# Optimization experiments

Hardware: AMD Instinct MI355X
Metric: run time of the kernel (lower is better)

Reference implementation:

```python
import jax, jax.numpy as jnp
import numpy as np

NU, NI, NR = 50000, 50000, 5   # users, items, rating levels
D, B, LS, LI = 64, 512, 32, 64 # embed_dim, batch, max social nbrs, max item hist
NEG = -1e9


def setup_inputs() -> dict:
    key = jax.random.key(0)
    ks = iter(jax.random.split(key, 64))
    def lin(din, dout):
        s = 1.0 / np.sqrt(din)
        return (jax.random.uniform(next(ks), (din, dout), minval=-s, maxval=s, dtype=jnp.float32),
                jax.random.uniform(next(ks), (dout,), minval=-s, maxval=s, dtype=jnp.float32))
    inp = {}
    inp['user_w'] = jax.random.normal(next(ks), (NU, D), dtype=jnp.float32) * 0.1
    inp['item_w'] = jax.random.normal(next(ks), (NI, D), dtype=jnp.float32) * 0.1
    inp['rating_w'] = jax.random.normal(next(ks), (NR, D), dtype=jnp.float32) * 0.1
    for name, din, dout in [('i_ln1', 2*D, D), ('i_ln2', D, D), ('i_ln3', 2*D, D),
                            ('i_att1', 2*D, D), ('i_att2', D, D), ('i_att3', D, 1),
                            ('s_ln1', D, D), ('s_ln2', 2*D, D), ('s_ln3', D, D),
                            ('s_att1', 2*D, D), ('s_att2', D, D), ('s_att3', D, 1)]:
        w, b = lin(din, dout)
        inp[name + '_w'] = w
        inp[name + '_b'] = b
    inp['nodes'] = jax.random.randint(next(ks), (B,), 0, NU)
    inp['social_hist'] = jax.random.randint(next(ks), (NU, LS), 0, NU)
    inp['social_mask'] = jax.random.bernoulli(next(ks), 0.5, (NU, LS)).at[:, 0].set(True)
    inp['item_hist'] = jax.random.randint(next(ks), (NU, LI), 0, NI)
    inp['rating_hist'] = jax.random.randint(next(ks), (NU, LI), 0, NR)
    inp['item_mask'] = jax.random.bernoulli(next(ks), 0.5, (NU, LI)).at[:, 0].set(True)
    return inp


def reference(user_w, item_w, rating_w,
              i_ln1_w, i_ln1_b, i_ln2_w, i_ln2_b, i_ln3_w, i_ln3_b,
              i_att1_w, i_att1_b, i_att2_w, i_att2_b, i_att3_w, i_att3_b,
              s_ln1_w, s_ln1_b, s_ln2_w, s_ln2_b, s_ln3_w, s_ln3_b,
              s_att1_w, s_att1_b, s_att2_w, s_att2_b, s_att3_w, s_att3_b,
              nodes, social_hist, social_mask, item_hist, rating_hist, item_mask):
    relu = jax.nn.relu

    def attn(x, w1, b1, w2, b2, w3, b3, mask):
        # x: [..., L, 2D] -> softmax weights over valid neighbors: [..., L]
        h = relu(x @ w1 + b1)
        h = relu(h @ w2 + b2)
        logit = (h @ w3 + b3)[..., 0]
        logit = jnp.where(mask, logit, NEG)
        return jax.nn.softmax(logit, axis=-1)

    def item_final(uids):
        # uids: any shape [...]; returns [..., D]  (Aggre_item.item_final)
        its, rts, m = item_hist[uids], rating_hist[uids], item_mask[uids]
        x = jnp.concatenate([item_w[its], rating_w[rts]], axis=-1)   # [...,LI,2D]
        x = relu(x @ i_ln1_w + i_ln1_b)                              # [...,LI,D]
        u = user_w[uids]                                             # [...,D]
        a_in = jnp.concatenate([x, jnp.broadcast_to(u[..., None, :], x.shape)], axis=-1)
        alpha = attn(a_in, i_att1_w, i_att1_b, i_att2_w, i_att2_b, i_att3_w, i_att3_b, m)
        hI = jnp.einsum('...l,...ld->...d', alpha, x)                # attention-weighted sum
        hI = relu(hI @ i_ln2_w + i_ln2_b)
        return relu(jnp.concatenate([u, hI], axis=-1) @ i_ln3_w + i_ln3_b)

    # item-space factor of query users
    hI_self = item_final(nodes)                                      # [B,D]
    # social aggregation: item_final over each user's social neighbors
    nbrs, nmask = social_hist[nodes], social_mask[nodes]             # [B,LS]
    hI_nb = item_final(nbrs)                                         # [B,LS,D]
    u = user_w[nodes]                                                # [B,D]
    b_in = jnp.concatenate([hI_nb, jnp.broadcast_to(u[:, None, :], hI_nb.shape)], axis=-1)
    beta = attn(b_in, s_att1_w, s_att1_b, s_att2_w, s_att2_b, s_att3_w, s_att3_b, nmask)
    hS = jnp.einsum('bl,bld->bd', beta, hI_nb)
    hS = relu(hS @ s_ln1_w + s_ln1_b)
    f = jnp.concatenate([hI_self, hS], axis=-1)
    f = relu(f @ s_ln2_w + s_ln2_b)
    return relu(f @ s_ln3_w + s_ln3_b)
```

## Files before the change

kernel.cpp:

```cpp
#include <hip/hip_runtime.h>
#include <math.h>


#define NII 50000
#define BB 512
#define LSS 32
#define NT 16896

typedef short short8 __attribute__((ext_vector_type(8)));
typedef float f32x4 __attribute__((ext_vector_type(4)));

static __device__ __forceinline__ bool mread(const void* p, long i, int mode) {
  if (mode == 0) return ((const int*)p)[i] != 0;
  if (mode == 2) return ((const float*)p)[i] != 0.0f;
  return ((const unsigned char*)p)[i] != 0;
}

static __device__ __forceinline__ float wsum(float v) {
#pragma unroll
  for (int s = 1; s < 64; s <<= 1) v += __shfl_xor(v, s);
  return v;
}
static __device__ __forceinline__ float wmax(float v) {
#pragma unroll
  for (int s = 1; s < 64; s <<= 1) v = fmaxf(v, __shfl_xor(v, s));
  return v;
}
static __device__ __forceinline__ float rsum16(float v) {
#pragma unroll
  for (int s = 1; s < 16; s <<= 1) v += __shfl_xor(v, s);
  return v;
}

static __device__ __forceinline__ short bf16rne(float f) {
  unsigned u = __float_as_uint(f);
  u = (u + 0x7FFFu + ((u >> 16) & 1u)) >> 16;
  return (short)u;
}
static __device__ __forceinline__ float bf16tof(short h) {
  return __uint_as_float(((unsigned)(unsigned short)h) << 16);
}

static __device__ __forceinline__ void wave_fence() {
  asm volatile("s_waitcnt lgkmcnt(0)" ::: "memory");
  __builtin_amdgcn_sched_barrier(0);
}

__global__ void setup_kernel(const unsigned int* __restrict__ sm,
                             int* __restrict__ flag,
                             const float* __restrict__ rating_w,
                             const float* __restrict__ w1,
                             const float* __restrict__ b1,
                             float* __restrict__ RW1g,
                             const float* __restrict__ A1w,
                             const float* __restrict__ A2w,
                             short* __restrict__ B1,
                             short* __restrict__ B2,
                             short* __restrict__ W1hi,
                             short* __restrict__ W1lo,
                             const int* __restrict__ nodes,
                             const int* __restrict__ social_hist,
                             int* __restrict__ counter,
                             int* __restrict__ list,
                             int* __restrict__ aUid) {
  const int tid = threadIdx.x;
  if (blockIdx.x == 0) {
    __shared__ int notInt, notFloat;
    if (tid == 0) { notInt = 0; notFloat = 0; }
    __syncthreads();
    int ni = 0, nf = 0;
    for (int i = tid; i < 4096; i += 256) {
      unsigned int x = sm[i];
      if (x > 1u) ni = 1;
      if (x != 0u && x != 0x3F800000u) nf = 1;
    }
    if (ni) atomicOr(&notInt, 1);
    if (nf) atomicOr(&notFloat, 1);
    __syncthreads();
    if (tid == 0) flag[0] = notInt ? (notFloat ? 1 : 2) : 0;
  } else if (blockIdx.x == 1) {
    for (int t = tid; t < 320; t += 256) {
      const int r = t >> 6, c = t & 63;
      float acc = b1[c];
      for (int k = 0; k < 64; ++k)
        acc = fmaf(rating_w[r * 64 + k], w1[(64 + k) * 64 + c], acc);
      RW1g[r * 64 + c] = acc;
    }
  } else if (blockIdx.x == 2) {
    for (int idx = tid; idx < 4096; idx += 256) {
      int e = idx & 7, g = idx >> 3;
      int l = g & 63, q = g >> 6;
      int kb = q >> 2, nb = q & 3;
      int k = kb * 32 + ((l >> 4) & 3) * 8 + e;
      int col = nb * 16 + (l & 15);
      B1[idx] = bf16rne(A1w[k * 64 + col]);
      B2[idx] = bf16rne(A2w[k * 64 + col]);
      float a = w1[k * 64 + col];
      short h = bf16rne(a);
      W1hi[idx] = h;
      W1lo[idx] = bf16rne(a - bf16tof(h));
    }
  } else {
    __shared__ int nI, nF;
    if (tid == 0) { nI = 0; nF = 0; }
    __syncthreads();
    int ni = 0, nf = 0;
    for (int i = tid; i < 4096; i += 256) {
      unsigned int x = sm[i];
      if (x > 1u) ni = 1;
      if (x != 0u && x != 0x3F800000u) nf = 1;
    }
    if (ni) atomicOr(&nI, 1);
    if (nf) atomicOr(&nF, 1);
    __syncthreads();
    const int mode = nI ? (nF ? 1 : 2) : 0;
    const int t = (blockIdx.x - 3) * 256 + tid;
    if (t < NT) {
      int uid;
      bool active;
      if (t < BB) {
        active = true;
        uid = nodes[t];
      } else {
        int nb = t - BB;
        int b = nb >> 5, l = nb & 31;
        long mi = (long)nodes[b] * LSS + l;
        active = mread((const void*)sm, mi, mode);
        uid = active ? social_hist[mi] : 0;
      }
      if (active) {
        int pos = atomicAdd(counter, 1);
        list[pos] = t;
        aUid[pos] = uid;
      }
    }
  }
}

__global__ __launch_bounds__(256)
void pre_xbase_mfma_kernel(const float* __restrict__ item_w,
                           const short* __restrict__ W1hi,
                           const short* __restrict__ W1lo,
                           float* __restrict__ xbase) {
  const int lane = threadIdx.x & 63, w = threadIdx.x >> 6;
  const int l15 = lane & 15, lg4 = lane >> 4;
  short8 bh[8], bl[8];
#pragma unroll
  for (int q = 0; q < 8; ++q) {
    bh[q] = *(const short8*)(W1hi + (q * 64 + lane) * 8);
    bl[q] = *(const short8*)(W1lo + (q * 64 + lane) * 8);
  }
  const int wid = blockIdx.x * 4 + w;
  const int nw = gridDim.x * 4;
  for (int tile = wid; tile < 3125; tile += nw) {
    const long r0 = (long)tile * 16;
    const float* ap = item_w + (r0 + l15) * 64 + lg4 * 8;
    short8 ah[2], al[2];
#pragma unroll
    for (int kb = 0; kb < 2; ++kb) {
      const float4 a = *(const float4*)(ap + kb * 32);
      const float4 b = *(const float4*)(ap + kb * 32 + 4);
      float v[8] = {a.x, a.y, a.z, a.w, b.x, b.y, b.z, b.w};
      short8 hi, lo;
#pragma unroll
      for (int e = 0; e < 8; ++e) {
        short h = bf16rne(v[e]);
        hi[e] = h;
        lo[e] = bf16rne(v[e] - bf16tof(h));
      }
      ah[kb] = hi;
      al[kb] = lo;
    }
#pragma unroll
    for (int nb = 0; nb < 4; ++nb) {
      f32x4 acc = {0.0f, 0.0f, 0.0f, 0.0f};
      acc = __builtin_amdgcn_mfma_f32_16x16x32_bf16(ah[0], bh[0 * 4 + nb], acc, 0, 0, 0);
      acc = __builtin_amdgcn_mfma_f32_16x16x32_bf16(ah[1], bh[1 * 4 + nb], acc, 0, 0, 0);
      acc = __builtin_amdgcn_mfma_f32_16x16x32_bf16(ah[0], bl[0 * 4 + nb], acc, 0, 0, 0);
      acc = __builtin_amdgcn_mfma_f32_16x16x32_bf16(ah[1], bl[1 * 4 + nb], acc, 0, 0, 0);
      acc = __builtin_amdgcn_mfma_f32_16x16x32_bf16(al[0], bh[0 * 4 + nb], acc, 0, 0, 0);
      acc = __builtin_amdgcn_mfma_f32_16x16x32_bf16(al[1], bh[1 * 4 + nb], acc, 0, 0, 0);
#pragma unroll
      for (int r = 0; r < 4; ++r)
        xbase[(r0 + lg4 * 4 + r) * 64 + nb * 16 + l15] = acc[r];
    }
  }
}

__global__ __launch_bounds__(256, 2)
void uA1_kernel(const float* __restrict__ user_w,
                const float* __restrict__ A1w, const float* __restrict__ A1b,
                const int* __restrict__ idxsrc, const int* __restrict__ nActp,
                float* __restrict__ uA1buf) {
  const int tid = threadIdx.x, lane = tid & 63, w = tid >> 6;
  const int i0 = blockIdx.x * 64;
  const int nA = nActp[0];
  if (i0 >= nA) return;
  __shared__ float sW[64][64], sU[64][64];
  __shared__ float sb[64];
  __shared__ int sUid[64];
  for (int i = tid; i < 4096; i += 256) sW[i >> 6][i & 63] = A1w[4096 + i];
  if (tid < 64) {
    sb[tid] = A1b[tid];
    sUid[tid] = (i0 + tid < nA) ? idxsrc[i0 + tid] : 0;
  }
  __syncthreads();
  for (int i = tid; i < 4096; i += 256) {
    int r = i >> 6, c = i & 63;
    sU[r][c] = user_w[(long)sUid[r] * 64 + c];
  }
  __syncthreads();
  float acc[16];
#pragma unroll
  for (int r = 0; r < 16; ++r) acc[r] = sb[lane];
  for (int k = 0; k < 64; k += 4) {
    float wv0 = sW[k][lane], wv1 = sW[k + 1][lane];
    float wv2 = sW[k + 2][lane], wv3 = sW[k + 3][lane];
#pragma unroll
    for (int r = 0; r < 16; ++r) {
      const float4 xv = *(const float4*)(&sU[w * 16 + r][k]);
      acc[r] = fmaf(xv.x, wv0, acc[r]);
      acc[r] = fmaf(xv.y, wv1, acc[r]);
      acc[r] = fmaf(xv.z, wv2, acc[r]);
      acc[r] = fmaf(xv.w, wv3, acc[r]);
    }
  }
#pragma unroll
  for (int r = 0; r < 16; ++r) {
    int row = i0 + w * 16 + r;
    if (row < nA) uA1buf[(long)row * 64 + lane] = acc[r];
  }
}

__global__ __launch_bounds__(512, 8)
void core_mfma_kernel(const float* __restrict__ xbase,
                      const float* __restrict__ RW1g,
                      const float* __restrict__ uA1buf,
                      const short* __restrict__ Bimg1,
                      const short* __restrict__ Bimg2,
                      const float* __restrict__ A2b,
                      const float* __restrict__ A3w,
                      const int* __restrict__ item_hist,
                      const int* __restrict__ rating_hist,
                      const void* __restrict__ item_mask,
                      const int* __restrict__ flagp,
                      const int* __restrict__ aUid,
                      const int* __restrict__ nActp,
                      float* __restrict__ hvecbuf) {
  __shared__ __align__(16) short sB1[4096], sB2[4096];
  __shared__ __align__(16) char smem[8][3072];
  const int tid = threadIdx.x, lane = tid & 63, w = tid >> 6;
  const int nA = nActp[0];
  if (blockIdx.x * 8 >= nA) return;

  short* h1w = (short*)(smem[w]);
  float* lgw = (float*)(smem[w] + 2560);
  int* cw = (int*)(smem[w] + 2816);

  ((int4*)sB1)[tid] = ((const int4*)Bimg1)[tid];
  ((int4*)sB2)[tid] = ((const int4*)Bimg2)[tid];
  __syncthreads();

  const int idx = blockIdx.x * 8 + w;
  if (idx >= nA) return;

  const int mode = flagp[0];
  const float a2bv = A2b[lane];
  const float a3v = A3w[lane];
  const int l15 = lane & 15;
  const int lg4 = lane >> 4;

#define B1F(q) (*(const short8*)(sB1 + ((q) * 64 + lane) * 8))
#define B2F(q) (*(const short8*)(sB2 + ((q) * 64 + lane) * 8))

  const long uid = aUid[idx];

  const long mbase = uid * 64;
  bool mk = mread(item_mask, mbase + lane, mode);
  unsigned long long bal = __ballot(mk);
  const int nact = (int)__popcll(bal);
  int pos = (int)__popcll(bal & ((1ull << lane) - 1ull));
  if (mk) cw[pos] = (item_hist[mbase + lane] << 3) | rating_hist[mbase + lane];
  const float uA1v = uA1buf[(long)idx * 64 + lane];
  wave_fence();

  const int ng = (nact + 15) >> 4;
  for (int mc = 0; mc < ng; ++mc) {
    wave_fence();
    int row = mc * 16 + l15;
    if (row >= nact) row = nact - 1;
    const int p = cw[row];
    const long it = p >> 3;
    const int rt = p & 7;
    short8 xa[2];
#pragma unroll
    for (int kb = 0; kb < 2; ++kb) {
      const int koff = kb * 32 + lg4 * 8;
      const float* xp = xbase + it * 64 + koff;
      const float* rp = RW1g + rt * 64 + koff;
      const float4 a = *(const float4*)xp;
      const float4 b = *(const float4*)(xp + 4);
      const float4 c = *(const float4*)rp;
      const float4 d = *(const float4*)(rp + 4);
      short8 f;
      f[0] = bf16rne(fmaxf(a.x + c.x, 0.0f));
      f[1] = bf16rne(fmaxf(a.y + c.y, 0.0f));
      f[2] = bf16rne(fmaxf(a.z + c.z, 0.0f));
      f[3] = bf16rne(fmaxf(a.w + c.w, 0.0f));
      f[4] = bf16rne(fmaxf(b.x + d.x, 0.0f));
      f[5] = bf16rne(fmaxf(b.y + d.y, 0.0f));
      f[6] = bf16rne(fmaxf(b.z + d.z, 0.0f));
      f[7] = bf16rne(fmaxf(b.w + d.w, 0.0f));
      xa[kb] = f;
    }
#pragma unroll
    for (int nb = 0; nb < 4; ++nb) {
      const float ui = __shfl(uA1v, nb * 16 + l15);
      f32x4 acc = {ui, ui, ui, ui};
      acc = __builtin_amdgcn_mfma_f32_16x16x32_bf16(xa[0], B1F(0 * 4 + nb), acc, 0, 0, 0);
      acc = __builtin_amdgcn_mfma_f32_16x16x32_bf16(xa[1], B1F(1 * 4 + nb), acc, 0, 0, 0);
#pragma unroll
      for (int r = 0; r < 4; ++r)
        h1w[(lg4 * 4 + r) * 80 + nb * 16 + l15] = bf16rne(fmaxf(acc[r], 0.0f));
    }
    wave_fence();
    short8 ha[2];
    ha[0] = *(const short8*)(h1w + l15 * 80 + lg4 * 8);
    ha[1] = *(const short8*)(h1w + l15 * 80 + 32 + lg4 * 8);
    float t0 = 0.0f, t1 = 0.0f, t2 = 0.0f, t3 = 0.0f;
#pragma unroll
    for (int nb = 0; nb < 4; ++nb) {
      const float b2 = __shfl(a2bv, nb * 16 + l15);
      f32x4 acc = {b2, b2, b2, b2};
      acc = __builtin_amdgcn_mfma_f32_16x16x32_bf16(ha[0], B2F(0 * 4 + nb), acc, 0, 0, 0);
      acc = __builtin_amdgcn_mfma_f32_16x16x32_bf16(ha[1], B2F(1 * 4 + nb), acc, 0, 0, 0);
      const float a3c = __shfl(a3v, nb * 16 + l15);
      t0 = fmaf(fmaxf(acc[0], 0.0f), a3c, t0);
      t1 = fmaf(fmaxf(acc[1], 0.0f), a3c, t1);
      t2 = fmaf(fmaxf(acc[2], 0.0f), a3c, t2);
      t3 = fmaf(fmaxf(acc[3], 0.0f), a3c, t3);
    }
    t0 = rsum16(t0); t1 = rsum16(t1); t2 = rsum16(t2); t3 = rsum16(t3);
    if (l15 == 0) {
      const int jb = mc * 16 + lg4 * 4;
      lgw[jb + 0] = t0;
      lgw[jb + 1] = t1;
      lgw[jb + 2] = t2;
      lgw[jb + 3] = t3;
    }
  }
  wave_fence();

  const bool valid = (lane < nact);
  float lv = valid ? lgw[lane] : -1e30f;
  float mx = wmax(lv);
  float e = valid ? __expf(lv - mx) : 0.0f;
  float s = wsum(e);
  const float alpha = e / s;

  float h0 = 0.0f, hA = 0.0f, hB = 0.0f, hC = 0.0f;
  int j = 0;
  for (; j + 3 < nact; j += 4) {
    const int p0 = cw[j], p1 = cw[j + 1], p2 = cw[j + 2], p3 = cw[j + 3];
    const float a0 = __shfl(alpha, j), a1 = __shfl(alpha, j + 1);
    const float a2 = __shfl(alpha, j + 2), a3 = __shfl(alpha, j + 3);
    const float x0 = xbase[(long)(p0 >> 3) * 64 + lane] + RW1g[(p0 & 7) * 64 + lane];
    const float x1 = xbase[(long)(p1 >> 3) * 64 + lane] + RW1g[(p1 & 7) * 64 + lane];
    const float x2 = xbase[(long)(p2 >> 3) * 64 + lane] + RW1g[(p2 & 7) * 64 + lane];
    const float x3 = xbase[(long)(p3 >> 3) * 64 + lane] + RW1g[(p3 & 7) * 64 + lane];
    h0 = fmaf(a0, fmaxf(x0, 0.0f), h0);
    hA = fmaf(a1, fmaxf(x1, 0.0f), hA);
    hB = fmaf(a2, fmaxf(x2, 0.0f), hB);
    hC = fmaf(a3, fmaxf(x3, 0.0f), hC);
  }
  for (; j < nact; ++j) {
    const int p = cw[j];
    const float aj = __shfl(alpha, j);
    const float xv = xbase[(long)(p >> 3) * 64 + lane] + RW1g[(p & 7) * 64 + lane];
    h0 = fmaf(aj, fmaxf(xv, 0.0f), h0);
  }
  hvecbuf[(long)idx * 64 + lane] = (h0 + hA) + (hB + hC);
#undef B1F
#undef B2F
}

__global__ __launch_bounds__(256, 2)
void hI2final_kernel(const float* __restrict__ hvecbuf,
                     const float* __restrict__ user_w,
                     const float* __restrict__ W2w, const float* __restrict__ W2b,
                     const float* __restrict__ W3w, const float* __restrict__ W3b,
                     const int* __restrict__ list, const int* __restrict__ aUid,
                     const int* __restrict__ nActp, float* __restrict__ hIbuf) {
  const int tid = threadIdx.x, lane = tid & 63, w = tid >> 6;
  const int i0 = blockIdx.x * 32;
  const int nA = nActp[0];
  if (i0 >= nA) return;
  __shared__ float sW[128][64];
  __shared__ float sX[32][128];
  __shared__ float sb[64];
  __shared__ int sUid[32], sInst[32];
  for (int i = tid; i < 4096; i += 256) sW[i >> 6][i & 63] = W2w[i];
  if (tid < 64) sb[tid] = W2b[tid];
  if (tid < 32) {
    bool ok = (i0 + tid) < nA;
    sUid[tid] = ok ? aUid[i0 + tid] : 0;
    sInst[tid] = ok ? list[i0 + tid] : 0;
  }
  __syncthreads();
  for (int i = tid; i < 2048; i += 256) {
    int r = i >> 6, c = i & 63;
    sX[r][64 + c] = (i0 + r < nA) ? hvecbuf[(long)(i0 + r) * 64 + c] : 0.0f;
    sX[r][c] = user_w[(long)sUid[r] * 64 + c];
  }
  __syncthreads();

  float acc[8];
  {
    const float bv = sb[lane];
#pragma unroll
    for (int r = 0; r < 8; ++r) acc[r] = bv;
    for (int k = 0; k < 64; k += 4) {
      float wv0 = sW[k][lane], wv1 = sW[k + 1][lane];
      float wv2 = sW[k + 2][lane], wv3 = sW[k + 3][lane];
#pragma unroll
      for (int r = 0; r < 8; ++r) {
        const float4 xv = *(const float4*)(&sX[w * 8 + r][64 + k]);
        acc[r] = fmaf(xv.x, wv0, acc[r]);
        acc[r] = fmaf(xv.y, wv1, acc[r]);
        acc[r] = fmaf(xv.z, wv2, acc[r]);
        acc[r] = fmaf(xv.w, wv3, acc[r]);
      }
    }
#pragma unroll
    for (int r = 0; r < 8; ++r) sX[w * 8 + r][64 + lane] = fmaxf(acc[r], 0.0f);
  }
  __syncthreads();
  for (int i = tid; i < 8192; i += 256) sW[i >> 6][i & 63] = W3w[i];
  if (tid < 64) sb[tid] = W3b[tid];
  __syncthreads();

  {
    const float bv = sb[lane];
#pragma unroll
    for (int r = 0; r < 8; ++r) acc[r] = bv;
    for (int k = 0; k < 128; k += 4) {
      float wv0 = sW[k][lane], wv1 = sW[k + 1][lane];
      float wv2 = sW[k + 2][lane], wv3 = sW[k + 3][lane];
#pragma unroll
      for (int r = 0; r < 8; ++r) {
        const float4 xv = *(const float4*)(&sX[w * 8 + r][k]);
        acc[r] = fmaf(xv.x, wv0, acc[r]);
        acc[r] = fmaf(xv.y, wv1, acc[r]);
        acc[r] = fmaf(xv.z, wv2, acc[r]);
        acc[r] = fmaf(xv.w, wv3, acc[r]);
      }
    }
#pragma unroll
    for (int r = 0; r < 8; ++r) {
      int row = i0 + w * 8 + r;
      if (row < nA)
        hIbuf[(long)sInst[w * 8 + r] * 64 + lane] = fmaxf(acc[r], 0.0f);
    }
  }
}

__global__ __launch_bounds__(256, 8)
void social_fused_kernel(const float* __restrict__ hIbuf,
                         const float* __restrict__ user_w,
                         const float* __restrict__ S1w,
                         const float* __restrict__ S1b,
                         const float* __restrict__ S2w,
                         const float* __restrict__ S2b,
                         const float* __restrict__ S3w,
                         const float* __restrict__ L1w, const float* __restrict__ L1b,
                         const float* __restrict__ L2w, const float* __restrict__ L2b,
                         const float* __restrict__ L3w, const float* __restrict__ L3b,
                         const int* __restrict__ nodes,
                         const void* __restrict__ social_mask,
                         const int* __restrict__ flagp,
                         float* __restrict__ out) {
  __shared__ __align__(16) short sB1[4096], sB2[4096];
  __shared__ __align__(16) char smem[4][3584];
  const int tid = threadIdx.x, lane = tid & 63, w = tid >> 6;
  short* h1w = (short*)(smem[w]);
  float* lgw = (float*)(smem[w] + 2560);
  int* cw = (int*)(smem[w] + 2816);
  float* vA = (float*)(smem[w] + 3072);
  float* vB = (float*)(smem[w] + 3328);

  for (int i = tid; i < 4096; i += 256) {
    int e = i & 7, g = i >> 3;
    int l = g & 63, q = g >> 6;
    int kb = q >> 2, nb = q & 3;
    int k = kb * 32 + ((l >> 4) & 3) * 8 + e;
    int col = nb * 16 + (l & 15);
    sB1[i] = bf16rne(S1w[k * 64 + col]);
    sB2[i] = bf16rne(S2w[k * 64 + col]);
  }
  __syncthreads();

  const int mode = flagp[0];
  const int l15 = lane & 15;
  const int lg4 = lane >> 4;
  const int b = blockIdx.x * 4 + w;
  const long uid = nodes[b];

  bool m = (lane < LSS) ? mread(social_mask, uid * LSS + lane, mode) : false;
  unsigned long long bal = __ballot(m);
  const int nval = (int)__popcll(bal);
  int pos = (int)__popcll(bal & ((1ull << lane) - 1ull));
  if (m) cw[pos] = lane;

  const float uv = user_w[uid * 64 + lane];
  float uA1v = S1b[lane];
#pragma unroll 8
  for (int k = 0; k < 64; ++k)
    uA1v = fmaf(__shfl(uv, k), S1w[(64 + k) * 64 + lane], uA1v);
  const float a2bv = S2b[lane];
  const float a3v = S3w[lane];
  wave_fence();

  const long hbase = 512L + (long)b * 32;
  const int ng = (nval + 15) >> 4;
  for (int mc = 0; mc < ng; ++mc) {
    wave_fence();
    int row = mc * 16 + l15;
    if (row >= nval) row = nval - 1;
    const long hrow = hbase + cw[row];
    short8 xa[2];
#pragma unroll
    for (int kb = 0; kb < 2; ++kb) {
      const float* xp = hIbuf + hrow * 64 + kb * 32 + lg4 * 8;
      const float4 a = *(const float4*)xp;
      const float4 bb = *(const float4*)(xp + 4);
      short8 f;
      f[0] = bf16rne(a.x);  f[1] = bf16rne(a.y);
      f[2] = bf16rne(a.z);  f[3] = bf16rne(a.w);
      f[4] = bf16rne(bb.x); f[5] = bf16rne(bb.y);
      f[6] = bf16rne(bb.z); f[7] = bf16rne(bb.w);
      xa[kb] = f;
    }
#pragma unroll
    for (int nb = 0; nb < 4; ++nb) {
      const float ui = __shfl(uA1v, nb * 16 + l15);
      f32x4 acc = {ui, ui, ui, ui};
      acc = __builtin_amdgcn_mfma_f32_16x16x32_bf16(
          xa[0], *(const short8*)(sB1 + ((0 * 4 + nb) * 64 + lane) * 8), acc, 0, 0, 0);
      acc = __builtin_amdgcn_mfma_f32_16x16x32_bf16(
          xa[1], *(const short8*)(sB1 + ((1 * 4 + nb) * 64 + lane) * 8), acc, 0, 0, 0);
#pragma unroll
      for (int r = 0; r < 4; ++r)
        h1w[(lg4 * 4 + r) * 80 + nb * 16 + l15] = bf16rne(fmaxf(acc[r], 0.0f));
    }
    wave_fence();
    short8 ha[2];
    ha[0] = *(const short8*)(h1w + l15 * 80 + lg4 * 8);
    ha[1] = *(const short8*)(h1w + l15 * 80 + 32 + lg4 * 8);
    float t0 = 0.0f, t1 = 0.0f, t2 = 0.0f, t3 = 0.0f;
#pragma unroll
    for (int nb = 0; nb < 4; ++nb) {
      const float b2 = __shfl(a2bv, nb * 16 + l15);
      f32x4 acc = {b2, b2, b2, b2};
      acc = __builtin_amdgcn_mfma_f32_16x16x32_bf16(
          ha[0], *(const short8*)(sB2 + ((0 * 4 + nb) * 64 + lane) * 8), acc, 0, 0, 0);
      acc = __builtin_amdgcn_mfma_f32_16x16x32_bf16(
          ha[1], *(const short8*)(sB2 + ((1 * 4 + nb) * 64 + lane) * 8), acc, 0, 0, 0);
      const float a3c = __shfl(a3v, nb * 16 + l15);
      t0 = fmaf(fmaxf(acc[0], 0.0f), a3c, t0);
      t1 = fmaf(fmaxf(acc[1], 0.0f), a3c, t1);
      t2 = fmaf(fmaxf(acc[2], 0.0f), a3c, t2);
      t3 = fmaf(fmaxf(acc[3], 0.0f), a3c, t3);
    }
    t0 = rsum16(t0); t1 = rsum16(t1); t2 = rsum16(t2); t3 = rsum16(t3);
    if (l15 == 0) {
      const int jb = mc * 16 + lg4 * 4;
      lgw[jb + 0] = t0;
      lgw[jb + 1] = t1;
      lgw[jb + 2] = t2;
      lgw[jb + 3] = t3;
    }
  }
  wave_fence();

  const bool valid = (lane < nval);
  float lv = valid ? lgw[lane] : -1e30f;
  float mx = wmax(lv);
  float e = valid ? __expf(lv - mx) : 0.0f;
  float s = wsum(e);
  const float beta = e / s;

  float hs = 0.0f;
  for (int j = 0; j < nval; ++j) {
    const float bj = __shfl(beta, j);
    hs = fmaf(bj, hIbuf[(hbase + cw[j]) * 64 + lane], hs);
  }

  vA[lane] = hs;
  wave_fence();
  float acc = L1b[lane];
#pragma unroll 8
  for (int k = 0; k < 64; ++k) acc = fmaf(vA[k], L1w[k * 64 + lane], acc);
  const float vecB = fmaxf(acc, 0.0f);
  const float selfv = hIbuf[(long)b * 64 + lane];
  wave_fence();
  vA[lane] = selfv;
  vB[lane] = vecB;
  wave_fence();
  acc = L2b[lane];
#pragma unroll 8
  for (int k = 0; k < 64; ++k) acc = fmaf(vA[k], L2w[k * 64 + lane], acc);
#pragma unroll 8
  for (int k = 0; k < 64; ++k) acc = fmaf(vB[k], L2w[(64 + k) * 64 + lane], acc);
  const float fv = fmaxf(acc, 0.0f);
  wave_fence();
  vA[lane] = fv;
  wave_fence();
  acc = L3b[lane];
#pragma unroll 8
  for (int k = 0; k < 64; ++k) acc = fmaf(vA[k], L3w[k * 64 + lane], acc);
  out[(long)b * 64 + lane] = fmaxf(acc, 0.0f);
}

extern "C" void kernel_launch(void* const* d_in, const int* in_sizes, int n_in,
                              void* d_out, int out_size, void* d_ws, size_t ws_size,
                              hipStream_t stream) {
  const float* user_w   = (const float*)d_in[0];
  const float* item_w   = (const float*)d_in[1];
  const float* rating_w = (const float*)d_in[2];
  const float* i_ln1_w  = (const float*)d_in[3];
  const float* i_ln1_b  = (const float*)d_in[4];
  const float* i_ln2_w  = (const float*)d_in[5];
  const float* i_ln2_b  = (const float*)d_in[6];
  const float* i_ln3_w  = (const float*)d_in[7];
  const float* i_ln3_b  = (const float*)d_in[8];
  const float* i_att1_w = (const float*)d_in[9];
  const float* i_att1_b = (const float*)d_in[10];
  const float* i_att2_w = (const float*)d_in[11];
  const float* i_att2_b = (const float*)d_in[12];
  const float* i_att3_w = (const float*)d_in[13];
  const float* i_att3_b = (const float*)d_in[14];
  const float* s_ln1_w  = (const float*)d_in[15];
  const float* s_ln1_b  = (const float*)d_in[16];
  const float* s_ln2_w  = (const float*)d_in[17];
  const float* s_ln2_b  = (const float*)d_in[18];
  const float* s_ln3_w  = (const float*)d_in[19];
  const float* s_ln3_b  = (const float*)d_in[20];
  const float* s_att1_w = (const float*)d_in[21];
  const float* s_att1_b = (const float*)d_in[22];
  const float* s_att2_w = (const float*)d_in[23];
  const float* s_att2_b = (const float*)d_in[24];
  const float* s_att3_w = (const float*)d_in[25];
  const float* s_att3_b = (const float*)d_in[26];
  const int*  nodes       = (const int*)d_in[27];
  const int*  social_hist = (const int*)d_in[28];
  const void* social_mask = d_in[29];
  const int*  item_hist   = (const int*)d_in[30];
  const int*  rating_hist = (const int*)d_in[31];
  const void* item_mask   = d_in[32];

  char* ws = (char*)d_ws;
  int*   flag    = (int*)(ws + 0);
  int*   counter = (int*)(ws + 256);
  int*   list    = (int*)(ws + 512);
  int*   aUid    = (int*)(ws + 68096);
  float* uA1buf  = (float*)(ws + 135680);
  float* hIbuf   = uA1buf;
  float* hvecbuf = (float*)(ws + 4461056);
  short* W1hi    = (short*)(ws + 4461056);
  short* W1lo    = (short*)(ws + 4469248);
  float* xbase   = (float*)(ws + 8786432);
  float* RW1g    = (float*)(ws + 21586432);
  short* Bimg1   = (short*)(ws + 21587712);
  short* Bimg2   = (short*)(ws + 21595904);

  hipMemsetAsync(counter, 0, 4, stream);
  setup_kernel<<<3 + NT / 256, 256, 0, stream>>>(
      (const unsigned int*)social_mask, flag,
      rating_w, i_ln1_w, i_ln1_b, RW1g,
      i_att1_w, i_att2_w, Bimg1, Bimg2, W1hi, W1lo,
      nodes, social_hist, counter, list, aUid);
  pre_xbase_mfma_kernel<<<512, 256, 0, stream>>>(item_w, W1hi, W1lo, xbase);
  uA1_kernel<<<NT / 64, 256, 0, stream>>>(user_w, i_att1_w, i_att1_b,
                                          aUid, counter, uA1buf);
  core_mfma_kernel<<<NT / 8, 512, 0, stream>>>(
      xbase, RW1g, uA1buf, Bimg1, Bimg2, i_att2_b, i_att3_w,
      item_hist, rating_hist, item_mask, flag, aUid, counter, hvecbuf);
  hI2final_kernel<<<NT / 32, 256, 0, stream>>>(
      hvecbuf, user_w, i_ln2_w, i_ln2_b, i_ln3_w, i_ln3_b,
      list, aUid, counter, hIbuf);
  social_fused_kernel<<<BB / 4, 256, 0, stream>>>(
      hIbuf, user_w, s_att1_w, s_att1_b, s_att2_w, s_att2_b, s_att3_w,
      s_ln1_w, s_ln1_b, s_ln2_w, s_ln2_b, s_ln3_w, s_ln3_b,
      nodes, social_mask, flag, (float*)d_out);
}
```

Baseline: 115.1 us.

## Merge xbase and uA1 kernels into one launch and store xbase as bf16

Combines the item projection precompute and the user attention-projection kernel into one launch, where block ranges select which branch runs. This removes a kernel launch and the serialization between two independent stages. The precomputed item projection table is now stored as bf16 instead of fp32, which halves its write traffic and the gather traffic in the core kernel. In exchange, the weighted-sum path that previously used fp32 xbase values loses precision.

```diff
diff --git a/kernel.cpp b/kernel.cpp
--- a/kernel.cpp
+++ b/kernel.cpp
@@ -137,103 +137,101 @@
   }
 }
 
-__global__ __launch_bounds__(256)
-void pre_xbase_mfma_kernel(const float* __restrict__ item_w,
-                           const short* __restrict__ W1hi,
-                           const short* __restrict__ W1lo,
-                           float* __restrict__ xbase) {
-  const int lane = threadIdx.x & 63, w = threadIdx.x >> 6;
-  const int l15 = lane & 15, lg4 = lane >> 4;
-  short8 bh[8], bl[8];
-#pragma unroll
-  for (int q = 0; q < 8; ++q) {
-    bh[q] = *(const short8*)(W1hi + (q * 64 + lane) * 8);
-    bl[q] = *(const short8*)(W1lo + (q * 64 + lane) * 8);
-  }
-  const int wid = blockIdx.x * 4 + w;
-  const int nw = gridDim.x * 4;
-  for (int tile = wid; tile < 3125; tile += nw) {
-    const long r0 = (long)tile * 16;
-    const float* ap = item_w + (r0 + l15) * 64 + lg4 * 8;
-    short8 ah[2], al[2];
-#pragma unroll
-    for (int kb = 0; kb < 2; ++kb) {
-      const float4 a = *(const float4*)(ap + kb * 32);
-      const float4 b = *(const float4*)(ap + kb * 32 + 4);
-      float v[8] = {a.x, a.y, a.z, a.w, b.x, b.y, b.z, b.w};
-      short8 hi, lo;
-#pragma unroll
-      for (int e = 0; e < 8; ++e) {
-        short h = bf16rne(v[e]);
-        hi[e] = h;
-        lo[e] = bf16rne(v[e] - bf16tof(h));
-      }
-      ah[kb] = hi;
-      al[kb] = lo;
-    }
-#pragma unroll
-    for (int nb = 0; nb < 4; ++nb) {
-      f32x4 acc = {0.0f, 0.0f, 0.0f, 0.0f};
-      acc = __builtin_amdgcn_mfma_f32_16x16x32_bf16(ah[0], bh[0 * 4 + nb], acc, 0, 0, 0);
-      acc = __builtin_amdgcn_mfma_f32_16x16x32_bf16(ah[1], bh[1 * 4 + nb], acc, 0, 0, 0);
-      acc = __builtin_amdgcn_mfma_f32_16x16x32_bf16(ah[0], bl[0 * 4 + nb], acc, 0, 0, 0);
-      acc = __builtin_amdgcn_mfma_f32_16x16x32_bf16(ah[1], bl[1 * 4 + nb], acc, 0, 0, 0);
-      acc = __builtin_amdgcn_mfma_f32_16x16x32_bf16(al[0], bh[0 * 4 + nb], acc, 0, 0, 0);
-      acc = __builtin_amdgcn_mfma_f32_16x16x32_bf16(al[1], bh[1 * 4 + nb], acc, 0, 0, 0);
-#pragma unroll
-      for (int r = 0; r < 4; ++r)
-        xbase[(r0 + lg4 * 4 + r) * 64 + nb * 16 + l15] = acc[r];
-    }
-  }
-}
-
 __global__ __launch_bounds__(256, 2)
-void uA1_kernel(const float* __restrict__ user_w,
+void mid_kernel(const float* __restrict__ item_w,
+                const short* __restrict__ W1hi,
+                const short* __restrict__ W1lo,
+                short* __restrict__ xbase16,
+                const float* __restrict__ user_w,
                 const float* __restrict__ A1w, const float* __restrict__ A1b,
-                const int* __restrict__ idxsrc, const int* __restrict__ nActp,
+                const int* __restrict__ aUid, const int* __restrict__ nActp,
                 float* __restrict__ uA1buf) {
   const int tid = threadIdx.x, lane = tid & 63, w = tid >> 6;
-  const int i0 = blockIdx.x * 64;
-  const int nA = nActp[0];
-  if (i0 >= nA) return;
-  __shared__ float sW[64][64], sU[64][64];
-  __shared__ float sb[64];
-  __shared__ int sUid[64];
-  for (int i = tid; i < 4096; i += 256) sW[i >> 6][i & 63] = A1w[4096 + i];
-  if (tid < 64) {
-    sb[tid] = A1b[tid];
-    sUid[tid] = (i0 + tid < nA) ? idxsrc[i0 + tid] : 0;
-  }
-  __syncthreads();
-  for (int i = tid; i < 4096; i += 256) {
-    int r = i >> 6, c = i & 63;
-    sU[r][c] = user_w[(long)sUid[r] * 64 + c];
-  }
-  __syncthreads();
-  float acc[16];
-#pragma unroll
-  for (int r = 0; r < 16; ++r) acc[r] = sb[lane];
-  for (int k = 0; k < 64; k += 4) {
-    float wv0 = sW[k][lane], wv1 = sW[k + 1][lane];
-    float wv2 = sW[k + 2][lane], wv3 = sW[k + 3][lane];
+  if (blockIdx.x < 512) {
+    const int l15 = lane & 15, lg4 = lane >> 4;
+    short8 bh[8], bl[8];
+#pragma unroll
+    for (int q = 0; q < 8; ++q) {
+      bh[q] = *(const short8*)(W1hi + (q * 64 + lane) * 8);
+      bl[q] = *(const short8*)(W1lo + (q * 64 + lane) * 8);
+    }
+    const int wid = blockIdx.x * 4 + w;
+    for (int tile = wid; tile < 3125; tile += 2048) {
+      const long r0 = (long)tile * 16;
+      const float* ap = item_w + (r0 + l15) * 64 + lg4 * 8;
+      short8 ah[2], al[2];
+#pragma unroll
+      for (int kb = 0; kb < 2; ++kb) {
+        const float4 a = *(const float4*)(ap + kb * 32);
+        const float4 b = *(const float4*)(ap + kb * 32 + 4);
+        float v[8] = {a.x, a.y, a.z, a.w, b.x, b.y, b.z, b.w};
+        short8 hi, lo;
+#pragma unroll
+        for (int e = 0; e < 8; ++e) {
+          short h = bf16rne(v[e]);
+          hi[e] = h;
+          lo[e] = bf16rne(v[e] - bf16tof(h));
+        }
+        ah[kb] = hi;
+        al[kb] = lo;
+      }
+#pragma unroll
+      for (int nb = 0; nb < 4; ++nb) {
+        f32x4 acc = {0.0f, 0.0f, 0.0f, 0.0f};
+        acc = __builtin_amdgcn_mfma_f32_16x16x32_bf16(ah[0], bh[0 * 4 + nb], acc, 0, 0, 0);
+        acc = __builtin_amdgcn_mfma_f32_16x16x32_bf16(ah[1], bh[1 * 4 + nb], acc, 0, 0, 0);
+        acc = __builtin_amdgcn_mfma_f32_16x16x32_bf16(ah[0], bl[0 * 4 + nb], acc, 0, 0, 0);
+        acc = __builtin_amdgcn_mfma_f32_16x16x32_bf16(ah[1], bl[1 * 4 + nb], acc, 0, 0, 0);
+        acc = __builtin_amdgcn_mfma_f32_16x16x32_bf16(al[0], bh[0 * 4 + nb], acc, 0, 0, 0);
+        acc = __builtin_amdgcn_mfma_f32_16x16x32_bf16(al[1], bh[1 * 4 + nb], acc, 0, 0, 0);
+#pragma unroll
+        for (int r = 0; r < 4; ++r)
+          xbase16[(r0 + lg4 * 4 + r) * 64 + nb * 16 + l15] = bf16rne(acc[r]);
+      }
+    }
+  } else {
+    const int i0 = (blockIdx.x - 512) * 64;
+    const int nA = nActp[0];
+    if (i0 >= nA) return;
+    __shared__ float sW[64][64], sU[64][64];
+    __shared__ float sb[64];
+    __shared__ int sUid[64];
+    for (int i = tid; i < 4096; i += 256) sW[i >> 6][i & 63] = A1w[4096 + i];
+    if (tid < 64) {
+      sb[tid] = A1b[tid];
+      sUid[tid] = (i0 + tid < nA) ? aUid[i0 + tid] : 0;
+    }
+    __syncthreads();
+    for (int i = tid; i < 4096; i += 256) {
+      int r = i >> 6, c = i & 63;
+      sU[r][c] = user_w[(long)sUid[r] * 64 + c];
+    }
+    __syncthreads();
+    float acc[16];
+#pragma unroll
+    for (int r = 0; r < 16; ++r) acc[r] = sb[lane];
+    for (int k = 0; k < 64; k += 4) {
+      float wv0 = sW[k][lane], wv1 = sW[k + 1][lane];
+      float wv2 = sW[k + 2][lane], wv3 = sW[k + 3][lane];
+#pragma unroll
+      for (int r = 0; r < 16; ++r) {
+        const float4 xv = *(const float4*)(&sU[w * 16 + r][k]);
+        acc[r] = fmaf(xv.x, wv0, acc[r]);
+        acc[r] = fmaf(xv.y, wv1, acc[r]);
+        acc[r] = fmaf(xv.z, wv2, acc[r]);
+        acc[r] = fmaf(xv.w, wv3, acc[r]);
+      }
+    }
 #pragma unroll
     for (int r = 0; r < 16; ++r) {
-      const float4 xv = *(const float4*)(&sU[w * 16 + r][k]);
-      acc[r] = fmaf(xv.x, wv0, acc[r]);
-      acc[r] = fmaf(xv.y, wv1, acc[r]);
-      acc[r] = fmaf(xv.z, wv2, acc[r]);
-      acc[r] = fmaf(xv.w, wv3, acc[r]);
-    }
-  }
-#pragma unroll
-  for (int r = 0; r < 16; ++r) {
-    int row = i0 + w * 16 + r;
-    if (row < nA) uA1buf[(long)row * 64 + lane] = acc[r];
+      int row = i0 + w * 16 + r;
+      if (row < nA) uA1buf[(long)row * 64 + lane] = acc[r];
+    }
   }
 }
 
 __global__ __launch_bounds__(512, 8)
-void core_mfma_kernel(const float* __restrict__ xbase,
+void core_mfma_kernel(const short* __restrict__ xb16,
                       const float* __restrict__ RW1g,
                       const float* __restrict__ uA1buf,
                       const short* __restrict__ Bimg1,
@@ -296,21 +294,19 @@
 #pragma unroll
     for (int kb = 0; kb < 2; ++kb) {
       const int koff = kb * 32 + lg4 * 8;
-      const float* xp = xbase + it * 64 + koff;
+      const short8 xb = *(const short8*)(xb16 + it * 64 + koff);
       const float* rp = RW1g + rt * 64 + koff;
-      const float4 a = *(const float4*)xp;
-      const float4 b = *(const float4*)(xp + 4);
       const float4 c = *(const float4*)rp;
       const float4 d = *(const float4*)(rp + 4);
       short8 f;
-      f[0] = bf16rne(fmaxf(a.x + c.x, 0.0f));
-      f[1] = bf16rne(fmaxf(a.y + c.y, 0.0f));
-      f[2] = bf16rne(fmaxf(a.z + c.z, 0.0f));
-      f[3] = bf16rne(fmaxf(a.w + c.w, 0.0f));
-      f[4] = bf16rne(fmaxf(b.x + d.x, 0.0f));
-      f[5] = bf16rne(fmaxf(b.y + d.y, 0.0f));
-      f[6] = bf16rne(fmaxf(b.z + d.z, 0.0f));
-      f[7] = bf16rne(fmaxf(b.w + d.w, 0.0f));
+      f[0] = bf16rne(fmaxf(bf16tof(xb[0]) + c.x, 0.0f));
+      f[1] = bf16rne(fmaxf(bf16tof(xb[1]) + c.y, 0.0f));
+      f[2] = bf16rne(fmaxf(bf16tof(xb[2]) + c.z, 0.0f));
+      f[3] = bf16rne(fmaxf(bf16tof(xb[3]) + c.w, 0.0f));
+      f[4] = bf16rne(fmaxf(bf16tof(xb[4]) + d.x, 0.0f));
+      f[5] = bf16rne(fmaxf(bf16tof(xb[5]) + d.y, 0.0f));
+      f[6] = bf16rne(fmaxf(bf16tof(xb[6]) + d.z, 0.0f));
+      f[7] = bf16rne(fmaxf(bf16tof(xb[7]) + d.w, 0.0f));
       xa[kb] = f;
     }
 #pragma unroll
@@ -364,10 +360,10 @@
     const int p0 = cw[j], p1 = cw[j + 1], p2 = cw[j + 2], p3 = cw[j + 3];
     const float a0 = __shfl(alpha, j), a1 = __shfl(alpha, j + 1);
     const float a2 = __shfl(alpha, j + 2), a3 = __shfl(alpha, j + 3);
-    const float x0 = xbase[(long)(p0 >> 3) * 64 + lane] + RW1g[(p0 & 7) * 64 + lane];
-    const float x1 = xbase[(long)(p1 >> 3) * 64 + lane] + RW1g[(p1 & 7) * 64 + lane];
-    const float x2 = xbase[(long)(p2 >> 3) * 64 + lane] + RW1g[(p2 & 7) * 64 + lane];
-    const float x3 = xbase[(long)(p3 >> 3) * 64 + lane] + RW1g[(p3 & 7) * 64 + lane];
+    const float x0 = bf16tof(xb16[(long)(p0 >> 3) * 64 + lane]) + RW1g[(p0 & 7) * 64 + lane];
+    const float x1 = bf16tof(xb16[(long)(p1 >> 3) * 64 + lane]) + RW1g[(p1 & 7) * 64 + lane];
+    const float x2 = bf16tof(xb16[(long)(p2 >> 3) * 64 + lane]) + RW1g[(p2 & 7) * 64 + lane];
+    const float x3 = bf16tof(xb16[(long)(p3 >> 3) * 64 + lane]) + RW1g[(p3 & 7) * 64 + lane];
     h0 = fmaf(a0, fmaxf(x0, 0.0f), h0);
     hA = fmaf(a1, fmaxf(x1, 0.0f), hA);
     hB = fmaf(a2, fmaxf(x2, 0.0f), hB);
@@ -376,7 +372,7 @@
   for (; j < nact; ++j) {
     const int p = cw[j];
     const float aj = __shfl(alpha, j);
-    const float xv = xbase[(long)(p >> 3) * 64 + lane] + RW1g[(p & 7) * 64 + lane];
+    const float xv = bf16tof(xb16[(long)(p >> 3) * 64 + lane]) + RW1g[(p & 7) * 64 + lane];
     h0 = fmaf(aj, fmaxf(xv, 0.0f), h0);
   }
   hvecbuf[(long)idx * 64 + lane] = (h0 + hA) + (hB + hC);
@@ -668,7 +664,7 @@
   float* hvecbuf = (float*)(ws + 4461056);
   short* W1hi    = (short*)(ws + 4461056);
   short* W1lo    = (short*)(ws + 4469248);
-  float* xbase   = (float*)(ws + 8786432);
+  short* xbase16 = (short*)(ws + 8786432);
   float* RW1g    = (float*)(ws + 21586432);
   short* Bimg1   = (short*)(ws + 21587712);
   short* Bimg2   = (short*)(ws + 21595904);
@@ -679,11 +675,11 @@
       rating_w, i_ln1_w, i_ln1_b, RW1g,
       i_att1_w, i_att2_w, Bimg1, Bimg2, W1hi, W1lo,
       nodes, social_hist, counter, list, aUid);
-  pre_xbase_mfma_kernel<<<512, 256, 0, stream>>>(item_w, W1hi, W1lo, xbase);
-  uA1_kernel<<<NT / 64, 256, 0, stream>>>(user_w, i_att1_w, i_att1_b,
-                                          aUid, counter, uA1buf);
+  mid_kernel<<<512 + NT / 64, 256, 0, stream>>>(
+      item_w, W1hi, W1lo, xbase16,
+      user_w, i_att1_w, i_att1_b, aUid, counter, uA1buf);
   core_mfma_kernel<<<NT / 8, 512, 0, stream>>>(
-      xbase, RW1g, uA1buf, Bimg1, Bimg2, i_att2_b, i_att3_w,
+      xbase16, RW1g, uA1buf, Bimg1, Bimg2, i_att2_b, i_att3_w,
       item_hist, rating_hist, item_mask, flag, aUid, counter, hvecbuf);
   hI2final_kernel<<<NT / 32, 256, 0, stream>>>(
       hvecbuf, user_w, i_ln2_w, i_ln2_b, i_ln3_w, i_ln3_b,
```

Result: faster. 105.9 us (-8.0%).
